# Optimization experiments

Hardware: AMD Instinct MI355X
Metric: run time of the kernel (lower is better)

The kernel has to match this reference:

```python
import jax, jax.numpy as jnp
import numpy as np

D_IN = 1024
D_OUT = 1024
NUM_HEADS = 16
HEAD_DIM = D_OUT // NUM_HEADS


def setup_inputs() -> dict:
    key = jax.random.key(0)
    ks = jax.random.split(key, 6)
    scale = 0.02
    x = jax.random.normal(ks[0], (4, 2048, D_IN), dtype=jnp.float32)
    Wq = jax.random.normal(ks[1], (D_IN, D_OUT), dtype=jnp.float32) * scale
    Wk = jax.random.normal(ks[2], (D_IN, D_OUT), dtype=jnp.float32) * scale
    Wv = jax.random.normal(ks[3], (D_IN, D_OUT), dtype=jnp.float32) * scale
    Wo = jax.random.normal(ks[4], (D_OUT, D_OUT), dtype=jnp.float32) * scale
    bo = jax.random.normal(ks[5], (D_OUT,), dtype=jnp.float32) * scale
    return {"x": x, "Wq": Wq, "Wk": Wk, "Wv": Wv, "Wo": Wo, "bo": bo}


def reference(x, Wq, Wk, Wv, Wo, bo):
    b, n, _ = x.shape
    # QKV projections -> [b, h, n, hd]
    def split_heads(t):
        return t.reshape(b, n, NUM_HEADS, HEAD_DIM).transpose(0, 2, 1, 3)
    q = split_heads(x @ Wq)
    k = split_heads(x @ Wk)
    v = split_heads(x @ Wv)
    # scaled causal attention scores [b, h, n, n]
    scores = jnp.einsum('bhqd,bhkd->bhqk', q, k) / jnp.sqrt(jnp.float32(HEAD_DIM))
    causal = jnp.tril(jnp.ones((n, n), dtype=bool))
    scores = jnp.where(causal, scores, -jnp.inf)
    attn = jax.nn.softmax(scores, axis=-1)
    # dropout p=0.0 -> identity
    ctx = jnp.einsum('bhqk,bhkd->bhqd', attn, v)  # [b, h, n, hd]
    ctx = ctx.transpose(0, 2, 1, 3).reshape(b, n, D_OUT)
    return ctx @ Wo + bo
```

## Files before the change

kernel.cpp:

```cpp
#include <hip/hip_runtime.h>
#include <hip/hip_bf16.h>

typedef __bf16 bf16;
typedef __attribute__((ext_vector_type(8))) __bf16 bf16x8;
typedef __attribute__((ext_vector_type(4))) __bf16 bf16x4;
typedef __attribute__((ext_vector_type(4))) float floatx4;

#define DM 1024
#define NH 16
#define HD 64
#define SEQ 2048
#define BATCH 4
#define MTOT (BATCH * SEQ)

#if __has_builtin(__builtin_amdgcn_exp2f)
#define EXP2(x) __builtin_amdgcn_exp2f(x)
#else
#define EXP2(x) exp2f(x)
#endif

#define GLDS(g, l) \
  __builtin_amdgcn_global_load_lds((const __attribute__((address_space(1))) void*)(g), \
                                   (__attribute__((address_space(3))) void*)(l), 16, 0, 0)

__global__ void cvt_f32_bf16(const float* __restrict__ in, bf16* __restrict__ out, int n4) {
  int i = blockIdx.x * 256 + threadIdx.x;
  if (i < n4) {
    float4 v = ((const float4*)in)[i];
    bf16x4 o;
    o[0] = (bf16)v.x; o[1] = (bf16)v.y; o[2] = (bf16)v.z; o[3] = (bf16)v.w;
    ((bf16x4*)out)[i] = o;
  }
}

__global__ void transpose_cvt4(const float* __restrict__ Wq, const float* __restrict__ Wk,
                               const float* __restrict__ Wv, const float* __restrict__ Wo,
                               bf16* __restrict__ Wqkvt, bf16* __restrict__ Wot) {
  __shared__ float tile[32][33];
  const float* W;
  bf16* Wt;
  int z = blockIdx.z;
  if (z == 0) { W = Wq; Wt = Wqkvt; }
  else if (z == 1) { W = Wk; Wt = Wqkvt + (size_t)DM * DM; }
  else if (z == 2) { W = Wv; Wt = Wqkvt + (size_t)2 * DM * DM; }
  else { W = Wo; Wt = Wot; }
  int n0 = blockIdx.x * 32, k0 = blockIdx.y * 32;
  int tx = threadIdx.x, ty = threadIdx.y;
#pragma unroll
  for (int j = 0; j < 32; j += 8)
    tile[ty + j][tx] = W[(size_t)(k0 + ty + j) * DM + n0 + tx];
  __syncthreads();
#pragma unroll
  for (int j = 0; j < 32; j += 8)
    Wt[(size_t)(n0 + ty + j) * DM + k0 + tx] = (bf16)tile[tx][ty + j];
}

#define BK 64

__global__ __launch_bounds__(256, 3) void gemm_qkv(const bf16* __restrict__ A,
                                                   const bf16* __restrict__ Bt,
                                                   bf16* __restrict__ Qb,
                                                   bf16* __restrict__ Kb,
                                                   bf16* __restrict__ Vt) {
  __shared__ __align__(16) bf16 Alds[128 * BK];
  __shared__ __align__(16) bf16 Blds[128 * BK];
  const int K = 1024;
  int m0 = blockIdx.x * 128;
  int n0 = blockIdx.y * 128;
  int tid = threadIdx.x;
  int wave = tid >> 6, lane = tid & 63;
  int wm = (wave & 1) * 64, wn = (wave >> 1) * 64;
  int lm = lane & 15, quad = lane >> 4;
  int lm7 = lm & 7;

  int cbase = wave * 64 + lane;
  const bf16* gA[4];
  const bf16* gB[4];
  bf16 *lA[4], *lB[4];
#pragma unroll
  for (int seg = 0; seg < 4; ++seg) {
    int c = seg * 256 + cbase;
    int row = c >> 3;
    int col8 = (c & 7) ^ (row & 7);
    gA[seg] = A + (size_t)(m0 + row) * K + col8 * 8;
    gB[seg] = Bt + (size_t)(n0 + row) * K + col8 * 8;
    lA[seg] = Alds + c * 8;
    lB[seg] = Blds + c * 8;
  }

  floatx4 acc[4][4] = {};
  for (int kt = 0; kt < K; kt += BK) {
    __syncthreads();
#pragma unroll
    for (int seg = 0; seg < 4; ++seg) {
      GLDS(gA[seg] + kt, lA[seg]);
      GLDS(gB[seg] + kt, lB[seg]);
    }
    __syncthreads();
#pragma unroll
    for (int ks = 0; ks < 2; ++ks) {
      int xk = (ks * 4 + quad) ^ lm7;
      bf16x8 af[4], bfr[4];
#pragma unroll
      for (int t = 0; t < 4; ++t) {
        af[t] = *(const bf16x8*)(Alds + (wm + t * 16 + lm) * BK + xk * 8);
        bfr[t] = *(const bf16x8*)(Blds + (wn + t * 16 + lm) * BK + xk * 8);
      }
#pragma unroll
      for (int i = 0; i < 4; ++i)
#pragma unroll
        for (int j = 0; j < 4; ++j)
          acc[i][j] = __builtin_amdgcn_mfma_f32_16x16x32_bf16(af[i], bfr[j], acc[i][j], 0, 0, 0);
    }
  }
#pragma unroll
  for (int i = 0; i < 4; ++i) {
#pragma unroll
    for (int j = 0; j < 4; ++j) {
#pragma unroll
      for (int r = 0; r < 4; ++r) {
        int R = m0 + wm + i * 16 + quad * 4 + r;
        int C = n0 + wn + j * 16 + lm;
        int b = R >> 11, n = R & 2047;
        int proj = C >> 10, c = C & 1023;
        int h = c >> 6, d = c & 63;
        int bh = b * NH + h;
        bf16 bv = (bf16)acc[i][j][r];
        if (proj == 0)
          Qb[((size_t)bh * SEQ + n) * HD + d] = bv;
        else if (proj == 1)
          Kb[((size_t)bh * SEQ + n) * HD + d] = bv;
        else
          Vt[((size_t)bh * HD + d) * SEQ + n] = bv;
      }
    }
  }
}

__global__ __launch_bounds__(256, 3) void gemm_out(const bf16* __restrict__ A,
                                                   const bf16* __restrict__ Bt,
                                                   const float* __restrict__ bias,
                                                   float* __restrict__ out) {
  __shared__ __align__(16) bf16 Alds[128 * BK];
  __shared__ __align__(16) bf16 Blds[128 * BK];
  const int K = 1024;
  int m0 = blockIdx.x * 128;
  int n0 = blockIdx.y * 128;
  int tid = threadIdx.x;
  int wave = tid >> 6, lane = tid & 63;
  int wm = (wave & 1) * 64, wn = (wave >> 1) * 64;
  int lm = lane & 15, quad = lane >> 4;
  int lm7 = lm & 7;

  int cbase = wave * 64 + lane;
  const bf16* gA[4];
  const bf16* gB[4];
  bf16 *lA[4], *lB[4];
#pragma unroll
  for (int seg = 0; seg < 4; ++seg) {
    int c = seg * 256 + cbase;
    int row = c >> 3;
    int col8 = (c & 7) ^ (row & 7);
    gA[seg] = A + (size_t)(m0 + row) * K + col8 * 8;
    gB[seg] = Bt + (size_t)(n0 + row) * K + col8 * 8;
    lA[seg] = Alds + c * 8;
    lB[seg] = Blds + c * 8;
  }

  floatx4 acc[4][4] = {};
  for (int kt = 0; kt < K; kt += BK) {
    __syncthreads();
#pragma unroll
    for (int seg = 0; seg < 4; ++seg) {
      GLDS(gA[seg] + kt, lA[seg]);
      GLDS(gB[seg] + kt, lB[seg]);
    }
    __syncthreads();
#pragma unroll
    for (int ks = 0; ks < 2; ++ks) {
      int xk = (ks * 4 + quad) ^ lm7;
      bf16x8 af[4], bfr[4];
#pragma unroll
      for (int t = 0; t < 4; ++t) {
        af[t] = *(const bf16x8*)(Alds + (wm + t * 16 + lm) * BK + xk * 8);
        bfr[t] = *(const bf16x8*)(Blds + (wn + t * 16 + lm) * BK + xk * 8);
      }
#pragma unroll
      for (int i = 0; i < 4; ++i)
#pragma unroll
        for (int j = 0; j < 4; ++j)
          acc[i][j] = __builtin_amdgcn_mfma_f32_16x16x32_bf16(af[i], bfr[j], acc[i][j], 0, 0, 0);
    }
  }
#pragma unroll
  for (int i = 0; i < 4; ++i)
#pragma unroll
    for (int j = 0; j < 4; ++j)
#pragma unroll
      for (int r = 0; r < 4; ++r) {
        int R = m0 + wm + i * 16 + quad * 4 + r;
        int C = n0 + wn + j * 16 + lm;
        out[(size_t)R * DM + C] = acc[i][j][r] + bias[C];
      }
}

__global__ __launch_bounds__(512, 2) void attn(const bf16* __restrict__ Qb,
                                               const bf16* __restrict__ Kb,
                                               const bf16* __restrict__ Vt,
                                               bf16* __restrict__ ctx) {
  __shared__ __align__(16) bf16 KV[4][4096];
  int blk = blockIdx.x;
  int xcd = blk & 7;
  int idx = blk >> 3;
  int bh = (idx & 7) * 8 + xcd;
  int pr = idx >> 3;
  int tid = threadIdx.x, wave = tid >> 6, lane = tid & 63;
  int qg = wave & 3, par = wave >> 2;
  int lm = lane & 15, quad = lane >> 4;
  int lm7 = lm & 7;
  const bf16* Qp = Qb + (size_t)bh * SEQ * HD;
  const bf16* Kp = Kb + (size_t)bh * SEQ * HD;
  const bf16* Vp = Vt + (size_t)bh * HD * SEQ;
  int b = bh >> 4, h = bh & 15;
  const float QSCALE = 0.125f * 1.4426950408889634f;

  int c = tid;
  int r = c >> 3, l = (c & 7) ^ (r & 7);
  const bf16* Kg = Kp + (size_t)r * HD + l * 8;
  const bf16* Vg = Vp + (size_t)r * SEQ + (l >> 2) * 32 + (l & 3) * 4;

  const bf16* Kl = KV[par];
  const bf16* Vl = KV[2 + par];

  bf16x8 ones;
#pragma unroll
  for (int j = 0; j < 8; ++j) ones[j] = (lm == 0) ? (bf16)1.0f : (bf16)0.0f;

  int xk0 = (quad ^ lm7) * 8;
  int xk1 = ((4 + quad) ^ lm7) * 8;

  float* cbuf = (float*)&KV[0][0];
  int cb = qg * 1088 + lane;

#pragma unroll 1
  for (int half = 0; half < 2; ++half) {
    int qt = half ? pr : 15 - pr;
    int q0 = qt * 128;
    int rowbase = q0 + qg * 32;
    int ns = qt + 1;

    bf16x8 qfA[2], qfB[2];
#pragma unroll
    for (int ks2 = 0; ks2 < 2; ++ks2) {
      bf16x8 qa = *(const bf16x8*)(Qp + (size_t)(rowbase + lm) * HD + ks2 * 32 + quad * 8);
      bf16x8 qb = *(const bf16x8*)(Qp + (size_t)(rowbase + 16 + lm) * HD + ks2 * 32 + quad * 8);
#pragma unroll
      for (int j = 0; j < 8; ++j) {
        qa[j] = (bf16)((float)qa[j] * QSCALE);
        qb[j] = (bf16)((float)qb[j] * QSCALE);
      }
      qfA[ks2] = qa;
      qfB[ks2] = qb;
    }

    floatx4 accA[4] = {}, accB[4] = {};
    floatx4 aclA = {}, aclB = {};

    if (half) __syncthreads();

    bf16x8 kr0 = *(const bf16x8*)(Kg);
    bf16x8 kr1 = *(const bf16x8*)(Kg + (size_t)64 * HD);
    bf16x4 v0a = *(const bf16x4*)(Vg),      v0b = *(const bf16x4*)(Vg + 16);
    bf16x4 v1a = *(const bf16x4*)(Vg + 64), v1b = *(const bf16x4*)(Vg + 80);
    *(bf16x8*)(KV[0] + c * 8) = kr0;
    *(bf16x8*)(KV[1] + c * 8) = kr1;
    *(bf16x4*)(KV[2] + c * 8) = v0a; *(bf16x4*)(KV[2] + c * 8 + 4) = v0b;
    *(bf16x4*)(KV[3] + c * 8) = v1a; *(bf16x4*)(KV[3] + c * 8 + 4) = v1b;

#pragma unroll 1
    for (int s = 0; s < ns; ++s) {
      __syncthreads();
      if (s + 1 < ns) {
        int kt = (2 * s + 2) * 64;
        kr0 = *(const bf16x8*)(Kg + (size_t)kt * HD);
        kr1 = *(const bf16x8*)(Kg + (size_t)(kt + 64) * HD);
        v0a = *(const bf16x4*)(Vg + kt);      v0b = *(const bf16x4*)(Vg + kt + 16);
        v1a = *(const bf16x4*)(Vg + kt + 64); v1b = *(const bf16x4*)(Vg + kt + 80);
      }
      int kv0 = (2 * s + par) * 64;

      if (kv0 <= rowbase + 31) {
        floatx4 stA[4] = {}, stB[4] = {};
#pragma unroll
        for (int mt = 0; mt < 4; ++mt) {
          const bf16* kr = Kl + (mt * 16 + lm) * 64;
          bf16x8 kf0 = *(const bf16x8*)(kr + xk0);
          bf16x8 kf1 = *(const bf16x8*)(kr + xk1);
          stA[mt] = __builtin_amdgcn_mfma_f32_16x16x32_bf16(kf0, qfA[0], stA[mt], 0, 0, 0);
          stA[mt] = __builtin_amdgcn_mfma_f32_16x16x32_bf16(kf1, qfA[1], stA[mt], 0, 0, 0);
          stB[mt] = __builtin_amdgcn_mfma_f32_16x16x32_bf16(kf0, qfB[0], stB[mt], 0, 0, 0);
          stB[mt] = __builtin_amdgcn_mfma_f32_16x16x32_bf16(kf1, qfB[1], stB[mt], 0, 0, 0);
        }

        bf16x8 pfA2[2], pfB2[2];
        if (kv0 + 63 <= rowbase) {
#pragma unroll
          for (int mt = 0; mt < 4; ++mt)
#pragma unroll
            for (int rr = 0; rr < 4; ++rr) {
              pfA2[mt >> 1][(mt & 1) * 4 + rr] = (bf16)EXP2(stA[mt][rr]);
              pfB2[mt >> 1][(mt & 1) * 4 + rr] = (bf16)EXP2(stB[mt][rr]);
            }
        } else {
          int qrelA = rowbase - kv0 + lm;
          int qrelB = qrelA + 16;
#pragma unroll
          for (int mt = 0; mt < 4; ++mt)
#pragma unroll
            for (int rr = 0; rr < 4; ++rr) {
              int kvrel = mt * 16 + quad * 4 + rr;
              float pa = EXP2(stA[mt][rr]);
              float pbv = EXP2(stB[mt][rr]);
              if (kvrel > qrelA) pa = 0.f;
              if (kvrel > qrelB) pbv = 0.f;
              pfA2[mt >> 1][(mt & 1) * 4 + rr] = (bf16)pa;
              pfB2[mt >> 1][(mt & 1) * 4 + rr] = (bf16)pbv;
            }
        }

#pragma unroll
        for (int ks = 0; ks < 2; ++ks) {
          int xv = ks ? xk1 : xk0;
          aclA = __builtin_amdgcn_mfma_f32_16x16x32_bf16(ones, pfA2[ks], aclA, 0, 0, 0);
          aclB = __builtin_amdgcn_mfma_f32_16x16x32_bf16(ones, pfB2[ks], aclB, 0, 0, 0);
#pragma unroll
          for (int db = 0; db < 4; ++db) {
            bf16x8 vf = *(const bf16x8*)(Vl + (db * 16 + lm) * 64 + xv);
            accA[db] = __builtin_amdgcn_mfma_f32_16x16x32_bf16(vf, pfA2[ks], accA[db], 0, 0, 0);
            accB[db] = __builtin_amdgcn_mfma_f32_16x16x32_bf16(vf, pfB2[ks], accB[db], 0, 0, 0);
          }
        }
      }

      if (s + 1 < ns) {
        __syncthreads();
        *(bf16x8*)(KV[0] + c * 8) = kr0;
        *(bf16x8*)(KV[1] + c * 8) = kr1;
        *(bf16x4*)(KV[2] + c * 8) = v0a; *(bf16x4*)(KV[2] + c * 8 + 4) = v0b;
        *(bf16x4*)(KV[3] + c * 8) = v1a; *(bf16x4*)(KV[3] + c * 8 + 4) = v1b;
      }
    }

    __syncthreads();
    if (par) {
#pragma unroll
      for (int db = 0; db < 4; ++db)
#pragma unroll
        for (int rr = 0; rr < 4; ++rr)
          cbuf[cb + (db * 4 + rr) * 64] = accA[db][rr];
      cbuf[cb + 1024] = aclA[0];
    }
    __syncthreads();
    float aA = aclA[0], aB = aclB[0];
    if (!par) {
#pragma unroll
      for (int db = 0; db < 4; ++db)
#pragma unroll
        for (int rr = 0; rr < 4; ++rr)
          accA[db][rr] += cbuf[cb + (db * 4 + rr) * 64];
      aA += cbuf[cb + 1024];
    }
    __syncthreads();
    if (par) {
#pragma unroll
      for (int db = 0; db < 4; ++db)
#pragma unroll
        for (int rr = 0; rr < 4; ++rr)
          cbuf[cb + (db * 4 + rr) * 64] = accB[db][rr];
      cbuf[cb + 1024] = aclB[0];
    }
    __syncthreads();
    if (!par) {
#pragma unroll
      for (int db = 0; db < 4; ++db)
#pragma unroll
        for (int rr = 0; rr < 4; ++rr)
          accB[db][rr] += cbuf[cb + (db * 4 + rr) * 64];
      aB += cbuf[cb + 1024];

      float linvA = 1.0f / __shfl(aA, lm, 64);
      float linvB = 1.0f / __shfl(aB, lm, 64);

      bf16* crowA = ctx + ((size_t)b * SEQ + rowbase + lm) * DM + h * 64;
      bf16* crowB = crowA + (size_t)16 * DM;
#pragma unroll
      for (int db = 0; db < 4; ++db) {
        bf16x4 oa, ob;
#pragma unroll
        for (int rr = 0; rr < 4; ++rr) {
          oa[rr] = (bf16)(accA[db][rr] * linvA);
          ob[rr] = (bf16)(accB[db][rr] * linvB);
        }
        *(bf16x4*)(crowA + db * 16 + quad * 4) = oa;
        *(bf16x4*)(crowB + db * 16 + quad * 4) = ob;
      }
    }
  }
}

extern "C" void kernel_launch(void* const* d_in, const int* in_sizes, int n_in,
                              void* d_out, int out_size, void* d_ws, size_t ws_size,
                              hipStream_t stream) {
  const float* x = (const float*)d_in[0];
  const float* Wq = (const float*)d_in[1];
  const float* Wk = (const float*)d_in[2];
  const float* Wv = (const float*)d_in[3];
  const float* Wo = (const float*)d_in[4];
  const float* bo = (const float*)d_in[5];
  float* out = (float*)d_out;

  bf16* ws = (bf16*)d_ws;
  bf16* xb = ws;
  bf16* Wqkvt = xb + (size_t)MTOT * DM;
  bf16* Wot = Wqkvt + (size_t)3 * DM * DM;
  bf16* Qb = Wot + (size_t)DM * DM;
  bf16* Kb = Qb + (size_t)BATCH * NH * SEQ * HD;
  bf16* Vtb = Kb + (size_t)BATCH * NH * SEQ * HD;
  bf16* ctx = xb;

  cvt_f32_bf16<<<(MTOT * DM / 4 + 255) / 256, 256, 0, stream>>>(x, xb, MTOT * DM / 4);
  transpose_cvt4<<<dim3(32, 32, 4), dim3(32, 8), 0, stream>>>(Wq, Wk, Wv, Wo, Wqkvt, Wot);
  gemm_qkv<<<dim3(MTOT / 128, 3 * DM / 128), 256, 0, stream>>>(xb, Wqkvt, Qb, Kb, Vtb);
  attn<<<512, 512, 0, stream>>>(Qb, Kb, Vtb, ctx);
  gemm_out<<<dim3(MTOT / 128, DM / 128), 256, 0, stream>>>(ctx, Wot, bo, out);
}
```

Measured before the change: 243.8 us.

## Double-buffer GEMMs with async LDS loads, 256x128 tiles and XCD-aware block mapping

```diff
diff --git a/kernel.cpp b/kernel.cpp
--- a/kernel.cpp
+++ b/kernel.cpp
@@ -22,6 +22,8 @@
 #define GLDS(g, l) \
   __builtin_amdgcn_global_load_lds((const __attribute__((address_space(1))) void*)(g), \
                                    (__attribute__((address_space(3))) void*)(l), 16, 0, 0)
+
+#define VMW(N) asm volatile("s_waitcnt vmcnt(" #N ")" ::: "memory")
 
 __global__ void cvt_f32_bf16(const float* __restrict__ in, bf16* __restrict__ out, int n4) {
   int i = blockIdx.x * 256 + threadIdx.x;
@@ -55,64 +57,84 @@
     Wt[(size_t)(n0 + ty + j) * DM + k0 + tx] = (bf16)tile[tx][ty + j];
 }
 
-#define BK 64
-
-__global__ __launch_bounds__(256, 3) void gemm_qkv(const bf16* __restrict__ A,
+
+#define GEMM_PRELUDE(APTR, BPTR)                                         \
+  const int K = 1024;                                                    \
+  int tid = threadIdx.x, wave = tid >> 6, lane = tid & 63;               \
+  int wm = (wave >> 1) * 64, wn = (wave & 1) * 64;                       \
+  int lm = lane & 15, quad = lane >> 4;                                  \
+  int arow = tid >> 2, asc = tid & 3;                                    \
+  int aswz = asc ^ ((arow >> 1) & 3);                                    \
+  const bf16* gA0 = (APTR) + (size_t)(m0 + arow) * K + aswz * 8;         \
+  const bf16* gA1 = gA0 + (size_t)128 * K;                               \
+  const bf16* gB0 = (BPTR) + (size_t)(n0 + arow) * K + aswz * 8;         \
+  int axs = (quad ^ (((wm + lm) >> 1) & 3)) * 8;                         \
+  int bxs = (quad ^ (((wn + lm) >> 1) & 3)) * 8;                         \
+  floatx4 acc[4][4] = {};
+
+#define STG(NA, NB, KT, KS) do {                                         \
+    GLDS(gA0 + (KT) + (KS) * 32, NA[KS] + tid * 8);                      \
+    GLDS(gA1 + (KT) + (KS) * 32, NA[KS] + 4096 + tid * 8);               \
+    GLDS(gB0 + (KT) + (KS) * 32, NB[KS] + tid * 8);                      \
+  } while (0)
+
+#define PH(CA, CB, KS, STG_STMT, W_STMT) do {                            \
+    bf16x8 af_[4], bq_[4];                                               \
+    _Pragma("unroll")                                                    \
+    for (int i_ = 0; i_ < 4; ++i_)                                       \
+      af_[i_] = *(const bf16x8*)(CA[KS] + (wm + i_ * 16 + lm) * 32 + axs); \
+    _Pragma("unroll")                                                    \
+    for (int j_ = 0; j_ < 4; ++j_)                                       \
+      bq_[j_] = *(const bf16x8*)(CB[KS] + (wn + j_ * 16 + lm) * 32 + bxs); \
+    STG_STMT;                                                            \
+    __builtin_amdgcn_s_barrier();                                        \
+    __builtin_amdgcn_s_setprio(1);                                       \
+    _Pragma("unroll")                                                    \
+    for (int i_ = 0; i_ < 4; ++i_)                                       \
+      _Pragma("unroll")                                                  \
+      for (int j_ = 0; j_ < 4; ++j_)                                     \
+        acc[i_][j_] = __builtin_amdgcn_mfma_f32_16x16x32_bf16(af_[i_], bq_[j_], acc[i_][j_], 0, 0, 0); \
+    __builtin_amdgcn_s_setprio(0);                                       \
+    W_STMT;                                                              \
+    __builtin_amdgcn_s_barrier();                                        \
+  } while (0)
+
+#define GEMM_KLOOP()                                                     \
+  STG(A0, B0, 0, 0);                                                     \
+  STG(A0, B0, 0, 1);                                                     \
+  VMW(3);                                                                \
+  __builtin_amdgcn_s_barrier();                                          \
+  _Pragma("unroll 1")                                                    \
+  for (int tp = 0; tp < 7; ++tp) {                                       \
+    int kt = tp * 128;                                                   \
+    PH(A0, B0, 0, STG(A1, B1, kt + 64, 0), VMW(3));                      \
+    PH(A0, B0, 1, STG(A1, B1, kt + 64, 1), VMW(3));                      \
+    PH(A1, B1, 0, STG(A0, B0, kt + 128, 0), VMW(3));                     \
+    PH(A1, B1, 1, STG(A0, B0, kt + 128, 1), VMW(3));                     \
+  }                                                                      \
+  PH(A0, B0, 0, STG(A1, B1, 960, 0), VMW(3));                            \
+  PH(A0, B0, 1, STG(A1, B1, 960, 1), VMW(3));                            \
+  PH(A1, B1, 0, ((void)0), VMW(0));                                      \
+  PH(A1, B1, 1, ((void)0), ((void)0));
+
+__global__ __launch_bounds__(512, 1) void gemm_qkv(const bf16* __restrict__ A,
                                                    const bf16* __restrict__ Bt,
                                                    bf16* __restrict__ Qb,
                                                    bf16* __restrict__ Kb,
                                                    bf16* __restrict__ Vt) {
-  __shared__ __align__(16) bf16 Alds[128 * BK];
-  __shared__ __align__(16) bf16 Blds[128 * BK];
-  const int K = 1024;
-  int m0 = blockIdx.x * 128;
-  int n0 = blockIdx.y * 128;
-  int tid = threadIdx.x;
-  int wave = tid >> 6, lane = tid & 63;
-  int wm = (wave & 1) * 64, wn = (wave >> 1) * 64;
-  int lm = lane & 15, quad = lane >> 4;
-  int lm7 = lm & 7;
-
-  int cbase = wave * 64 + lane;
-  const bf16* gA[4];
-  const bf16* gB[4];
-  bf16 *lA[4], *lB[4];
-#pragma unroll
-  for (int seg = 0; seg < 4; ++seg) {
-    int c = seg * 256 + cbase;
-    int row = c >> 3;
-    int col8 = (c & 7) ^ (row & 7);
-    gA[seg] = A + (size_t)(m0 + row) * K + col8 * 8;
-    gB[seg] = Bt + (size_t)(n0 + row) * K + col8 * 8;
-    lA[seg] = Alds + c * 8;
-    lB[seg] = Blds + c * 8;
-  }
-
-  floatx4 acc[4][4] = {};
-  for (int kt = 0; kt < K; kt += BK) {
-    __syncthreads();
-#pragma unroll
-    for (int seg = 0; seg < 4; ++seg) {
-      GLDS(gA[seg] + kt, lA[seg]);
-      GLDS(gB[seg] + kt, lB[seg]);
-    }
-    __syncthreads();
-#pragma unroll
-    for (int ks = 0; ks < 2; ++ks) {
-      int xk = (ks * 4 + quad) ^ lm7;
-      bf16x8 af[4], bfr[4];
-#pragma unroll
-      for (int t = 0; t < 4; ++t) {
-        af[t] = *(const bf16x8*)(Alds + (wm + t * 16 + lm) * BK + xk * 8);
-        bfr[t] = *(const bf16x8*)(Blds + (wn + t * 16 + lm) * BK + xk * 8);
-      }
-#pragma unroll
-      for (int i = 0; i < 4; ++i)
-#pragma unroll
-        for (int j = 0; j < 4; ++j)
-          acc[i][j] = __builtin_amdgcn_mfma_f32_16x16x32_bf16(af[i], bfr[j], acc[i][j], 0, 0, 0);
-    }
-  }
+  __shared__ __align__(16) bf16 A0[2][8192];
+  __shared__ __align__(16) bf16 A1[2][8192];
+  __shared__ __align__(16) bf16 B0[2][4096];
+  __shared__ __align__(16) bf16 B1[2][4096];
+  int bid = blockIdx.x;
+  int xcd = bid & 7, idx = bid >> 3;
+  int rm = xcd >> 1, rn = xcd & 1;
+  int mt = rm * 8 + (idx & 7);
+  int nt = rn * 12 + (idx >> 3);
+  int m0 = mt * 256, n0 = nt * 128;
+  GEMM_PRELUDE(A, Bt)
+  GEMM_KLOOP()
+
 #pragma unroll
   for (int i = 0; i < 4; ++i) {
 #pragma unroll
@@ -137,61 +159,22 @@
   }
 }
 
-__global__ __launch_bounds__(256, 3) void gemm_out(const bf16* __restrict__ A,
+__global__ __launch_bounds__(512, 1) void gemm_out(const bf16* __restrict__ A,
                                                    const bf16* __restrict__ Bt,
                                                    const float* __restrict__ bias,
                                                    float* __restrict__ out) {
-  __shared__ __align__(16) bf16 Alds[128 * BK];
-  __shared__ __align__(16) bf16 Blds[128 * BK];
-  const int K = 1024;
-  int m0 = blockIdx.x * 128;
-  int n0 = blockIdx.y * 128;
-  int tid = threadIdx.x;
-  int wave = tid >> 6, lane = tid & 63;
-  int wm = (wave & 1) * 64, wn = (wave >> 1) * 64;
-  int lm = lane & 15, quad = lane >> 4;
-  int lm7 = lm & 7;
-
-  int cbase = wave * 64 + lane;
-  const bf16* gA[4];
-  const bf16* gB[4];
-  bf16 *lA[4], *lB[4];
-#pragma unroll
-  for (int seg = 0; seg < 4; ++seg) {
-    int c = seg * 256 + cbase;
-    int row = c >> 3;
-    int col8 = (c & 7) ^ (row & 7);
-    gA[seg] = A + (size_t)(m0 + row) * K + col8 * 8;
-    gB[seg] = Bt + (size_t)(n0 + row) * K + col8 * 8;
-    lA[seg] = Alds + c * 8;
-    lB[seg] = Blds + c * 8;
-  }
-
-  floatx4 acc[4][4] = {};
-  for (int kt = 0; kt < K; kt += BK) {
-    __syncthreads();
-#pragma unroll
-    for (int seg = 0; seg < 4; ++seg) {
-      GLDS(gA[seg] + kt, lA[seg]);
-      GLDS(gB[seg] + kt, lB[seg]);
-    }
-    __syncthreads();
-#pragma unroll
-    for (int ks = 0; ks < 2; ++ks) {
-      int xk = (ks * 4 + quad) ^ lm7;
-      bf16x8 af[4], bfr[4];
-#pragma unroll
-      for (int t = 0; t < 4; ++t) {
-        af[t] = *(const bf16x8*)(Alds + (wm + t * 16 + lm) * BK + xk * 8);
-        bfr[t] = *(const bf16x8*)(Blds + (wn + t * 16 + lm) * BK + xk * 8);
-      }
-#pragma unroll
-      for (int i = 0; i < 4; ++i)
-#pragma unroll
-        for (int j = 0; j < 4; ++j)
-          acc[i][j] = __builtin_amdgcn_mfma_f32_16x16x32_bf16(af[i], bfr[j], acc[i][j], 0, 0, 0);
-    }
-  }
+  __shared__ __align__(16) bf16 A0[2][8192];
+  __shared__ __align__(16) bf16 A1[2][8192];
+  __shared__ __align__(16) bf16 B0[2][4096];
+  __shared__ __align__(16) bf16 B1[2][4096];
+  int bid = blockIdx.x;
+  int xcd = bid & 7, idx = bid >> 3;
+  int mt = xcd * 4 + (idx & 3);
+  int nt = idx >> 2;
+  int m0 = mt * 256, n0 = nt * 128;
+  GEMM_PRELUDE(A, Bt)
+  GEMM_KLOOP()
+
 #pragma unroll
   for (int i = 0; i < 4; ++i)
 #pragma unroll
@@ -430,7 +413,7 @@
 
   cvt_f32_bf16<<<(MTOT * DM / 4 + 255) / 256, 256, 0, stream>>>(x, xb, MTOT * DM / 4);
   transpose_cvt4<<<dim3(32, 32, 4), dim3(32, 8), 0, stream>>>(Wq, Wk, Wv, Wo, Wqkvt, Wot);
-  gemm_qkv<<<dim3(MTOT / 128, 3 * DM / 128), 256, 0, stream>>>(xb, Wqkvt, Qb, Kb, Vtb);
+  gemm_qkv<<<768, 512, 0, stream>>>(xb, Wqkvt, Qb, Kb, Vtb);
   attn<<<512, 512, 0, stream>>>(Qb, Kb, Vtb, ctx);
-  gemm_out<<<dim3(MTOT / 128, DM / 128), 256, 0, stream>>>(ctx, Wot, bo, out);
-}
+  gemm_out<<<256, 512, 0, stream>>>(ctx, Wot, bo, out);
+}
```

Measured after the change: 283.0 us. 16.1% more time.
